# Kernel tuning notes

Hardware: AMD Instinct MI355X
Metric: run time of the kernel (lower is better)

Reference implementation:

```python
import jax, jax.numpy as jnp
import numpy as np

FEATURE_DIM = 4
H_PATCHES = 16
W_PATCHES = 16
PATCH_H = 16
PATCH_W = 16
D = FEATURE_DIM * PATCH_H * PATCH_W  # 1024
N = 2 * H_PATCHES * W_PATCHES        # 512
M = 256
B = 64
EPS = 1e-5


def layernorm(x, g, b):
    mu = jnp.mean(x, axis=-1, keepdims=True)
    var = jnp.var(x, axis=-1, keepdims=True)
    return (x - mu) * jax.lax.rsqrt(var + EPS) * g + b


def box3x3(x):
    # per-channel 3x3 window sum with zero padding == diagonal conv in BCIM
    p = jnp.pad(x, ((0, 0), (0, 0), (1, 1), (1, 1)))
    H, W = x.shape[2], x.shape[3]
    return sum(p[:, :, i:i + H, j:j + W] for i in range(3) for j in range(3))


def setup_inputs() -> dict:
    key = jax.random.key(0)
    ks = jax.random.split(key, 20)
    rn = lambda k, shp, s=0.02: (jax.random.normal(k, shp, dtype=jnp.float32) * s)
    inp = {
        'p_vector': jax.random.normal(ks[0], (B, N, D), dtype=jnp.float32),
        'object_vector': jax.random.normal(ks[1], (M, D), dtype=jnp.float32),
        'ln_p_g': 1.0 + rn(ks[2], (D,), 0.1), 'ln_p_b': rn(ks[3], (D,)),
        'ln_o_g': 1.0 + rn(ks[4], (D,), 0.1), 'ln_o_b': rn(ks[5], (D,)),
        'Wq': rn(ks[6], (D, D)), 'bq': rn(ks[7], (D,)),
        'Wk': rn(ks[8], (D, D)), 'bk': rn(ks[9], (D,)),
        'Wv': rn(ks[10], (D, D)), 'bv': rn(ks[11], (D,)),
        'W1': rn(ks[12], (D, D)), 'b1': rn(ks[13], (D,)),
        'ln1_g': 1.0 + rn(ks[14], (D,), 0.1), 'ln1_b': rn(ks[15], (D,)),
        'W2': rn(ks[16], (D, D)), 'b2': rn(ks[17], (D,)),
        'ln2_g': 1.0 + rn(ks[18], (D,), 0.1), 'ln2_b': rn(ks[19], (D,)),
    }
    return inp


def reference(p_vector, object_vector, ln_p_g, ln_p_b, ln_o_g, ln_o_b,
              Wq, bq, Wk, bk, Wv, bv, W1, b1, ln1_g, ln1_b,
              W2, b2, ln2_g, ln2_b):
    # cross-attention (single head, full D)
    p = layernorm(p_vector, ln_p_g, ln_p_b)            # [B,N,D]
    o = layernorm(object_vector, ln_o_g, ln_o_b)       # [M,D]
    q = jnp.einsum('bnd,de->bne', p, Wq) + bq
    k = o @ Wk + bk                                    # [M,D]
    v = o @ Wv + bv
    A = jax.nn.softmax(jnp.einsum('bnd,md->bnm', q, k), axis=-1)
    p = p + jnp.einsum('bnm,md->bnd', A, v)
    # projection block: Linear->LN->GELU->Linear->LN->GELU, residual
    h = jax.nn.gelu(layernorm(jnp.einsum('bnd,de->bne', p, W1) + b1, ln1_g, ln1_b), approximate=False)
    h = jax.nn.gelu(layernorm(jnp.einsum('bnd,de->bne', h, W2) + b2, ln2_g, ln2_b), approximate=False)
    p = p + h
    # BCIM: reshape to image of 2D channels
    x = jnp.transpose(p, (0, 2, 1)).reshape(B, 2 * D, H_PATCHES, W_PATCHES)
    norm = jnp.linalg.norm(x, axis=1, keepdims=True)
    unit = x / norm
    win = box3x3(unit) / 9.0
    sim = jnp.sum(unit * win, axis=1, keepdims=True)   # [B,1,hp,wp]
    x = x * sim
    # reshape back to [B, 2*hp*wp, D]
    x = jnp.transpose(x, (0, 2, 3, 1)).reshape(B, H_PATCHES, W_PATCHES, D, 2)
    x = jnp.transpose(x, (0, 4, 1, 2, 3)).reshape(B, 2 * H_PATCHES * W_PATCHES, D)
    return x
```

## Files before the change

### kernel.cpp

```cpp
#include <hip/hip_runtime.h>
#include <math.h>

#define D_DIM 1024
#define M_DIM 256
#define B_IMG 64
#define N_TOK 512
#define BN    32768

typedef unsigned short u16;
typedef __attribute__((ext_vector_type(8))) __bf16 bf16x8;
typedef __attribute__((ext_vector_type(4))) float  f32x4;

__device__ __forceinline__ u16 f2bf(float f) {
  union { float f; unsigned u; } c; c.f = f;
  unsigned u = c.u;
  return (u16)((u + 0x7FFFu + ((u >> 16) & 1u)) >> 16);
}
__device__ __forceinline__ float bf2f(u16 h) {
  union { unsigned u; float f; } c; c.u = ((unsigned)h) << 16;
  return c.f;
}

__global__ __launch_bounds__(64) void detect_dtype(const u16* __restrict__ p, int* __restrict__ dflag)
{
  const int lane = threadIdx.x;
  const float a = fabsf(bf2f(p[lane * 2]));
  const bool sane = (a >= 1e-20f && a <= 1e3f);
  const unsigned long long m = __ballot(sane);
  if (lane == 0) *dflag = (m == ~0ull) ? 0 : 1;
}

__device__ __forceinline__ float load_in(const void* p, size_t i, int f) {
  return f ? ((const float*)p)[i] : bf2f(((const u16*)p)[i]);
}

template<int EPI>
__global__ __launch_bounds__(256) void gemm_bt(
    const u16* __restrict__ X0, const u16* __restrict__ X1, const u16* __restrict__ X2,
    const u16* __restrict__ Bt0, const u16* __restrict__ Bt1, const u16* __restrict__ Bt2,
    const void* __restrict__ bias, const int* __restrict__ dflag,
    int np_base, int np_extra,
    const u16* res_hi, const u16* res_lo,
    float* outf, u16* outb, u16* outb2,
    int R, int K, int NC)
{
  __shared__ u16 lA[128 * 64];
  __shared__ u16 lB[128 * 64];
  const int tid  = threadIdx.x;
  const int wave = tid >> 6, lane = tid & 63;
  const int quad = lane >> 4, l15 = lane & 15;
  const int wr = wave & 1, wc = wave >> 1;
  const int rblk = blockIdx.x, cblk = blockIdx.y;

  const int np = np_base + (np_extra ? np_extra * (*dflag) : 0);

  const int srow = lane >> 3;
  const int scol = ((lane & 7) ^ (srow & 7)) * 8;

  const u16* Xs[3] = {X0, X1, X2};
  const u16* Bs[3] = {Bt0, Bt1, Bt2};

  f32x4 acc[4][4] = {};

  for (int p = 0; p < np; ++p) {
    const u16* gA = Xs[p] + (size_t)(rblk * 128 + srow) * K + scol;
    const u16* gB = Bs[p] + (size_t)(cblk * 128 + srow) * K + scol;
    for (int k0 = 0; k0 < K; k0 += 64) {
#pragma unroll
      for (int i = 0; i < 4; ++i) {
        const int j = i * 4 + wave;
        __builtin_amdgcn_global_load_lds(
            (const __attribute__((address_space(1))) void*)(gA + (size_t)j * 8 * K + k0),
            (__attribute__((address_space(3))) void*)(lA + j * 512), 16, 0, 0);
        __builtin_amdgcn_global_load_lds(
            (const __attribute__((address_space(1))) void*)(gB + (size_t)j * 8 * K + k0),
            (__attribute__((address_space(3))) void*)(lB + j * 512), 16, 0, 0);
      }
      __syncthreads();
#pragma unroll
      for (int s = 0; s < 2; ++s) {
        bf16x8 af[4], bfr[4];
#pragma unroll
        for (int r = 0; r < 4; ++r) {
          const int row  = wr * 64 + r * 16 + l15;
          const int slot = (s * 4 + quad) ^ (row & 7);
          af[r] = *(const bf16x8*)(lA + row * 64 + slot * 8);
        }
#pragma unroll
        for (int c = 0; c < 4; ++c) {
          const int row  = wc * 64 + c * 16 + l15;
          const int slot = (s * 4 + quad) ^ (row & 7);
          bfr[c] = *(const bf16x8*)(lB + row * 64 + slot * 8);
        }
#pragma unroll
        for (int r = 0; r < 4; ++r)
#pragma unroll
          for (int c = 0; c < 4; ++c)
            acc[r][c] = __builtin_amdgcn_mfma_f32_16x16x32_bf16(af[r], bfr[c], acc[r][c], 0, 0, 0);
      }
      __syncthreads();
    }
  }

  const int fdt = bias ? *dflag : 0;
  const int crow0 = rblk * 128 + wr * 64;
  const int ccol0 = cblk * 128 + wc * 64;
#pragma unroll
  for (int c = 0; c < 4; ++c) {
    const int col = ccol0 + c * 16 + l15;
    const float bcol = bias ? load_in(bias, col, fdt) : 0.0f;
#pragma unroll
    for (int r = 0; r < 4; ++r) {
#pragma unroll
      for (int t = 0; t < 4; ++t) {
        const int row = crow0 + r * 16 + quad * 4 + t;
        const size_t idx = (size_t)row * NC + col;
        float v = acc[r][c][t] + bcol;
        if (EPI == 0) {
          outb[idx] = f2bf(v);
        } else if (EPI == 1) {
          outf[idx] = v;
        } else if (EPI == 2) {
          const float p = bf2f(res_hi[idx]) + bf2f(res_lo[idx]) + v;
          const u16 hi = f2bf(p);
          outb[idx]  = hi;
          outb2[idx] = f2bf(p - bf2f(hi));
        } else if (EPI == 3) {
          outb[(size_t)col * R + row] = f2bf(v);
        } else {
          const u16 hi = f2bf(v);
          outb[idx]  = hi;
          outb2[idx] = f2bf(v - bf2f(hi));
        }
      }
    }
  }
}

template<int EPI>
__global__ __launch_bounds__(512, 2) void gemm256(
    const u16* __restrict__ X0, const u16* __restrict__ X1, const u16* __restrict__ X2,
    const u16* __restrict__ Bt0, const u16* __restrict__ Bt1, const u16* __restrict__ Bt2,
    const void* __restrict__ bias, const int* __restrict__ dflag,
    int np_base, int np_extra,
    const u16* res_hi, const u16* res_lo,
    float* outf, u16* outb, u16* outb2,
    int R, int K, int NC)
{
  extern __shared__ u16 lds2[];
  const int tid  = threadIdx.x;
  const int wave = tid >> 6, lane = tid & 63;
  const int quad = lane >> 4, l15 = lane & 15;
  const int wm = wave >> 2, wn = wave & 3;
  const int rblk = blockIdx.x, cblk = blockIdx.y;

  const int np = np_base + (np_extra ? np_extra * (*dflag) : 0);
  const int ktiles = K >> 5;
  const int ktl = 31 - __builtin_clz(ktiles);
  const int NT = np << ktl;

  const u16* Xs[3] = {X0, X1, X2};
  const u16* Bs[3] = {Bt0, Bt1, Bt2};

  const int srow  = lane >> 2;
  const int sslot = lane & 3;

  f32x4 acc[8][4] = {};

  auto stage_tile = [&](int t) {
    const int tc = t < NT ? t : NT - 1;
    const int p  = tc >> ktl;
    const int k0 = (tc & (ktiles - 1)) << 5;
    u16* dst = lds2 + (t & 3) * 16384;
#pragma unroll
    for (int i = 0; i < 2; ++i) {
      const int rbase = wave * 32 + i * 16;
      const int r  = rbase + srow;
      const int cg = (sslot ^ ((r >> 1) & 3)) * 8;
      __builtin_amdgcn_global_load_lds(
          (const __attribute__((address_space(1))) void*)(Xs[p] + (size_t)(rblk * 256 + r) * K + k0 + cg),
          (__attribute__((address_space(3))) void*)(dst + rbase * 32), 16, 0, 0);
    }
#pragma unroll
    for (int i = 0; i < 2; ++i) {
      const int rbase = wave * 32 + i * 16;
      const int r  = rbase + srow;
      const int cg = (sslot ^ ((r >> 1) & 3)) * 8;
      __builtin_amdgcn_global_load_lds(
          (const __attribute__((address_space(1))) void*)(Bs[p] + (size_t)(cblk * 256 + r) * K + k0 + cg),
          (__attribute__((address_space(3))) void*)(dst + 8192 + rbase * 32), 16, 0, 0);
    }
  };

  stage_tile(0);
  stage_tile(1);
  asm volatile("s_waitcnt vmcnt(4)" ::: "memory");
  __builtin_amdgcn_s_barrier();

  for (int t = 0; t < NT; ++t) {
    const u16* bufA = lds2 + (t & 3) * 16384;
    const u16* bufB = bufA + 8192;
    bf16x8 bfr[4], af[4];
#pragma unroll
    for (int n = 0; n < 4; ++n) {
      const int row = wn * 64 + n * 16 + l15;
      const int ps  = quad ^ ((row >> 1) & 3);
      bfr[n] = *(const bf16x8*)(bufB + row * 32 + ps * 8);
    }
#pragma unroll
    for (int m = 0; m < 4; ++m) {
      const int row = wm * 128 + m * 16 + l15;
      const int ps  = quad ^ ((row >> 1) & 3);
      af[m] = *(const bf16x8*)(bufA + row * 32 + ps * 8);
    }
    stage_tile(t + 2);
    __builtin_amdgcn_s_barrier();
    asm volatile("s_waitcnt lgkmcnt(0)" ::: "memory");
    __builtin_amdgcn_s_setprio(1);
#pragma unroll
    for (int m = 0; m < 4; ++m)
#pragma unroll
      for (int n = 0; n < 4; ++n)
        acc[m][n] = __builtin_amdgcn_mfma_f32_16x16x32_bf16(af[m], bfr[n], acc[m][n], 0, 0, 0);
    __builtin_amdgcn_s_setprio(0);
    __builtin_amdgcn_s_barrier();
#pragma unroll
    for (int m = 0; m < 4; ++m) {
      const int row = wm * 128 + 64 + m * 16 + l15;
      const int ps  = quad ^ ((row >> 1) & 3);
      af[m] = *(const bf16x8*)(bufA + row * 32 + ps * 8);
    }
    asm volatile("s_waitcnt vmcnt(4)" ::: "memory");
    __builtin_amdgcn_s_barrier();
    asm volatile("s_waitcnt lgkmcnt(0)" ::: "memory");
    __builtin_amdgcn_s_setprio(1);
#pragma unroll
    for (int m = 0; m < 4; ++m)
#pragma unroll
      for (int n = 0; n < 4; ++n)
        acc[4 + m][n] = __builtin_amdgcn_mfma_f32_16x16x32_bf16(af[m], bfr[n], acc[4 + m][n], 0, 0, 0);
    __builtin_amdgcn_s_setprio(0);
    __builtin_amdgcn_s_barrier();
  }

  const int fdt = bias ? *dflag : 0;
  const int crow0 = rblk * 256 + wm * 128;
  const int ccol0 = cblk * 256 + wn * 64;
#pragma unroll
  for (int n = 0; n < 4; ++n) {
    const int col = ccol0 + n * 16 + l15;
    const float bcol = bias ? load_in(bias, col, fdt) : 0.0f;
#pragma unroll
    for (int m = 0; m < 8; ++m) {
#pragma unroll
      for (int u = 0; u < 4; ++u) {
        const int row = crow0 + m * 16 + quad * 4 + u;
        const size_t idx = (size_t)row * NC + col;
        float v = acc[m][n][u] + bcol;
        if (EPI == 0) {
          outb[idx] = f2bf(v);
        } else if (EPI == 1) {
          outf[idx] = v;
        } else if (EPI == 2) {
          const float pp = bf2f(res_hi[idx]) + bf2f(res_lo[idx]) + v;
          const u16 hi = f2bf(pp);
          outb[idx]  = hi;
          outb2[idx] = f2bf(pp - bf2f(hi));
        } else {
          const u16 hi = f2bf(v);
          outb[idx]  = hi;
          outb2[idx] = f2bf(v - bf2f(hi));
        }
      }
    }
  }
}

__global__ __launch_bounds__(256) void ln_row(
    const void* __restrict__ x, const void* __restrict__ g, const void* __restrict__ b,
    const int* __restrict__ dflag, u16* __restrict__ oh, u16* __restrict__ ol)
{
  const int f = *dflag;
  const int row = blockIdx.x, tid = threadIdx.x;
  const int col = tid * 4;
  const size_t base = (size_t)row * 1024 + col;
  float v0, v1, v2, v3;
  if (f) {
    const float4 xv = *(const float4*)((const float*)x + base);
    v0 = xv.x; v1 = xv.y; v2 = xv.z; v3 = xv.w;
  } else {
    const ushort4 xv = *(const ushort4*)((const u16*)x + base);
    v0 = bf2f(xv.x); v1 = bf2f(xv.y); v2 = bf2f(xv.z); v3 = bf2f(xv.w);
  }
  float s  = v0 + v1 + v2 + v3;
  float sq = v0 * v0 + v1 * v1 + v2 * v2 + v3 * v3;
#pragma unroll
  for (int o = 32; o > 0; o >>= 1) { s += __shfl_xor(s, o); sq += __shfl_xor(sq, o); }
  __shared__ float red[8];
  if ((tid & 63) == 0) { red[tid >> 6] = s; red[4 + (tid >> 6)] = sq; }
  __syncthreads();
  s  = red[0] + red[1] + red[2] + red[3];
  sq = red[4] + red[5] + red[6] + red[7];
  const float mean = s * (1.0f / 1024.0f);
  const float var  = sq * (1.0f / 1024.0f) - mean * mean;
  const float rs   = rsqrtf(var + 1e-5f);
  float y[4];
  y[0] = (v0 - mean) * rs * load_in(g, col + 0, f) + load_in(b, col + 0, f);
  y[1] = (v1 - mean) * rs * load_in(g, col + 1, f) + load_in(b, col + 1, f);
  y[2] = (v2 - mean) * rs * load_in(g, col + 2, f) + load_in(b, col + 2, f);
  y[3] = (v3 - mean) * rs * load_in(g, col + 3, f) + load_in(b, col + 3, f);
  ushort4 hv, lv;
  hv.x = f2bf(y[0]); lv.x = f2bf(y[0] - bf2f(hv.x));
  hv.y = f2bf(y[1]); lv.y = f2bf(y[1] - bf2f(hv.y));
  hv.z = f2bf(y[2]); lv.z = f2bf(y[2] - bf2f(hv.z));
  hv.w = f2bf(y[3]); lv.w = f2bf(y[3] - bf2f(hv.w));
  *(ushort4*)(oh + base) = hv;
  *(ushort4*)(ol + base) = lv;
}

template<int MODE>
__global__ __launch_bounds__(256) void ln_gelu(
    const u16* __restrict__ x, const void* __restrict__ g, const void* __restrict__ b,
    const int* __restrict__ dflag,
    const u16* res_hi, const u16* res_lo,
    u16* ob, u16* oh, u16* ol)
{
  const int f = *dflag;
  const int row = blockIdx.x, tid = threadIdx.x;
  const int col = tid * 4;
  const size_t base = (size_t)row * 1024 + col;
  const ushort4 xv = *(const ushort4*)(x + base);
  const float v0 = bf2f(xv.x), v1 = bf2f(xv.y), v2 = bf2f(xv.z), v3 = bf2f(xv.w);
  float s  = v0 + v1 + v2 + v3;
  float sq = v0 * v0 + v1 * v1 + v2 * v2 + v3 * v3;
#pragma unroll
  for (int o = 32; o > 0; o >>= 1) { s += __shfl_xor(s, o); sq += __shfl_xor(sq, o); }
  __shared__ float red[8];
  if ((tid & 63) == 0) { red[tid >> 6] = s; red[4 + (tid >> 6)] = sq; }
  __syncthreads();
  s  = red[0] + red[1] + red[2] + red[3];
  sq = red[4] + red[5] + red[6] + red[7];
  const float mean = s * (1.0f / 1024.0f);
  const float var  = sq * (1.0f / 1024.0f) - mean * mean;
  const float rs   = rsqrtf(var + 1e-5f);
  float z[4], h[4];
  z[0] = (v0 - mean) * rs * load_in(g, col + 0, f) + load_in(b, col + 0, f);
  z[1] = (v1 - mean) * rs * load_in(g, col + 1, f) + load_in(b, col + 1, f);
  z[2] = (v2 - mean) * rs * load_in(g, col + 2, f) + load_in(b, col + 2, f);
  z[3] = (v3 - mean) * rs * load_in(g, col + 3, f) + load_in(b, col + 3, f);
#pragma unroll
  for (int i = 0; i < 4; ++i)
    h[i] = 0.5f * z[i] * (1.0f + erff(z[i] * 0.70710678118654752f));
  if (MODE == 0) {
    *(ushort4*)(ob + base) = make_ushort4(f2bf(h[0]), f2bf(h[1]), f2bf(h[2]), f2bf(h[3]));
  } else {
    const ushort4 rh = *(const ushort4*)(res_hi + base);
    const ushort4 rl = *(const ushort4*)(res_lo + base);
    float p[4];
    p[0] = bf2f(rh.x) + bf2f(rl.x) + h[0];
    p[1] = bf2f(rh.y) + bf2f(rl.y) + h[1];
    p[2] = bf2f(rh.z) + bf2f(rl.z) + h[2];
    p[3] = bf2f(rh.w) + bf2f(rl.w) + h[3];
    ushort4 hv, lv;
    hv.x = f2bf(p[0]); lv.x = f2bf(p[0] - bf2f(hv.x));
    hv.y = f2bf(p[1]); lv.y = f2bf(p[1] - bf2f(hv.y));
    hv.z = f2bf(p[2]); lv.z = f2bf(p[2] - bf2f(hv.z));
    hv.w = f2bf(p[3]); lv.w = f2bf(p[3] - bf2f(hv.w));
    *(ushort4*)(oh + base) = hv;
    *(ushort4*)(ol + base) = lv;
  }
}

__global__ __launch_bounds__(256) void softmax256(const float* __restrict__ S, u16* __restrict__ A)
{
  const int tid = threadIdx.x, lane = tid & 63, wave = tid >> 6;
  const size_t row = (size_t)blockIdx.x * 4 + wave;
  const float4 v = *(const float4*)(S + row * 256 + lane * 4);
  float m = fmaxf(fmaxf(v.x, v.y), fmaxf(v.z, v.w));
#pragma unroll
  for (int o = 32; o > 0; o >>= 1) m = fmaxf(m, __shfl_xor(m, o));
  const float e0 = expf(v.x - m), e1 = expf(v.y - m), e2 = expf(v.z - m), e3 = expf(v.w - m);
  float s = e0 + e1 + e2 + e3;
#pragma unroll
  for (int o = 32; o > 0; o >>= 1) s += __shfl_xor(s, o);
  const float r = 1.0f / s;
  *(ushort4*)(A + row * 256 + lane * 4) =
      make_ushort4(f2bf(e0 * r), f2bf(e1 * r), f2bf(e2 * r), f2bf(e3 * r));
}

__global__ __launch_bounds__(256) void wtrans5(
    const void* w0, const void* w1, const void* w2, const void* w3, const void* w4,
    u16* h0, u16* h1, u16* h2, u16* h3, u16* h4,
    u16* l0, u16* l1, u16* l2, u16* l3, u16* l4,
    const int* __restrict__ dflag)
{
  const int f = *dflag;
  const void* W; u16* H; u16* L;
  switch (blockIdx.z) {
    case 0: W = w0; H = h0; L = l0; break;
    case 1: W = w1; H = h1; L = l1; break;
    case 2: W = w2; H = h2; L = l2; break;
    case 3: W = w3; H = h3; L = l3; break;
    default: W = w4; H = h4; L = l4; break;
  }
  __shared__ u16 th[32][33];
  __shared__ u16 tl[32][33];
  const int tx = threadIdx.x & 31, ty = threadIdx.x >> 5;
  const int bx = blockIdx.x, by = blockIdx.y;
#pragma unroll
  for (int i = 0; i < 4; ++i) {
    const int r = ty + i * 8;
    const float v = load_in(W, ((size_t)by * 32 + r) * 1024 + bx * 32 + tx, f);
    const u16 hi = f2bf(v);
    th[r][tx] = hi;
    tl[r][tx] = f2bf(v - bf2f(hi));
  }
  __syncthreads();
#pragma unroll
  for (int i = 0; i < 4; ++i) {
    const int r = ty + i * 8;
    const size_t o = ((size_t)bx * 32 + r) * 1024 + by * 32 + tx;
    H[o] = th[tx][r];
    L[o] = tl[tx][r];
  }
}

__global__ __launch_bounds__(256) void zerof(float* p, int n)
{
  const int i = blockIdx.x * 256 + threadIdx.x;
  if (i < n) p[i] = 0.0f;
}

__global__ __launch_bounds__(256) void bcim_dots(
    const u16* __restrict__ p2h, const u16* __restrict__ p2l, float* __restrict__ G)
{
  const int b = blockIdx.x, ds = blockIdx.y;
  __shared__ float T[512][17];
  float acc[9] = {0, 0, 0, 0, 0, 0, 0, 0, 0};
  const int tid = threadIdx.x;
  const int px = tid & 15, py = tid >> 4;
  for (int ch = 0; ch < 8; ++ch) {
    const int d0 = ds * 128 + ch * 16;
#pragma unroll
    for (int i = 0; i < 8; ++i) {
      const int j = i * 256 + tid;
      const int r = j >> 2, q4 = j & 3;
      const size_t base = ((size_t)b * 512 + r) * 1024 + d0 + q4 * 4;
      const ushort4 hv = *(const ushort4*)(p2h + base);
      const ushort4 lv = *(const ushort4*)(p2l + base);
      T[r][q4 * 4 + 0] = bf2f(hv.x) + bf2f(lv.x);
      T[r][q4 * 4 + 1] = bf2f(hv.y) + bf2f(lv.y);
      T[r][q4 * 4 + 2] = bf2f(hv.z) + bf2f(lv.z);
      T[r][q4 * 4 + 3] = bf2f(hv.w) + bf2f(lv.w);
    }
    __syncthreads();
    float a0[16], a1[16];
#pragma unroll
    for (int dc = 0; dc < 16; ++dc) { a0[dc] = T[tid][dc]; a1[dc] = T[tid + 256][dc]; }
#pragma unroll
    for (int o = 0; o < 9; ++o) {
      const int dy = o / 3 - 1, dx = o % 3 - 1;
      const int qx = px + dx, qy = py + dy;
      if (qx >= 0 && qx < 16 && qy >= 0 && qy < 16) {
        const int qp = qy * 16 + qx;
        float sum = 0.0f;
#pragma unroll
        for (int dc = 0; dc < 16; ++dc)
          sum += a0[dc] * T[qp][dc] + a1[dc] * T[qp + 256][dc];
        acc[o] += sum;
      }
    }
    __syncthreads();
  }
#pragma unroll
  for (int o = 0; o < 9; ++o)
    atomicAdd(&G[((size_t)b * 9 + o) * 256 + tid], acc[o]);
}

__global__ __launch_bounds__(256) void bcim_sim_k(const float* __restrict__ G, float* __restrict__ sim)
{
  const int b = blockIdx.x, tid = threadIdx.x;
  __shared__ float nrm[256];
  const float nv = sqrtf(G[((size_t)b * 9 + 4) * 256 + tid]);
  nrm[tid] = nv;
  __syncthreads();
  const int px = tid & 15, py = tid >> 4;
  float s = 0.0f;
#pragma unroll
  for (int o = 0; o < 9; ++o) {
    const int dy = o / 3 - 1, dx = o % 3 - 1;
    const int qx = px + dx, qy = py + dy;
    if (qx >= 0 && qx < 16 && qy >= 0 && qy < 16)
      s += G[((size_t)b * 9 + o) * 256 + tid] / (nv * nrm[qy * 16 + qx]);
  }
  sim[b * 256 + tid] = s * (1.0f / 9.0f);
}

__global__ __launch_bounds__(256) void bcim_scale(
    const u16* __restrict__ p2h, const u16* __restrict__ p2l,
    const float* __restrict__ sim, float* __restrict__ out)
{
  const size_t i4 = (size_t)blockIdx.x * 256 + threadIdx.x;
  const size_t base = i4 * 4;
  const ushort4 hv = *(const ushort4*)(p2h + base);
  const ushort4 lv = *(const ushort4*)(p2l + base);
  const size_t n = base >> 10;
  const size_t b = n >> 9;
  const int pix = (int)(n & 255);
  const float s = sim[b * 256 + pix];
  *(float4*)(out + base) = make_float4(
      (bf2f(hv.x) + bf2f(lv.x)) * s, (bf2f(hv.y) + bf2f(lv.y)) * s,
      (bf2f(hv.z) + bf2f(lv.z)) * s, (bf2f(hv.w) + bf2f(lv.w)) * s);
}

extern "C" void kernel_launch(void* const* d_in, const int* in_sizes, int n_in,
                              void* d_out, int out_size, void* d_ws, size_t ws_size,
                              hipStream_t stream)
{
  (void)in_sizes; (void)n_in; (void)out_size; (void)ws_size;
  const void* p_vector      = d_in[0];
  const void* object_vector = d_in[1];
  const void* ln_p_g = d_in[2];
  const void* ln_p_b = d_in[3];
  const void* ln_o_g = d_in[4];
  const void* ln_o_b = d_in[5];
  const void* Wq = d_in[6];  const void* bq = d_in[7];
  const void* Wk = d_in[8];  const void* bk = d_in[9];
  const void* Wv = d_in[10]; const void* bv = d_in[11];
  const void* W1 = d_in[12]; const void* b1 = d_in[13];
  const void* ln1_g = d_in[14]; const void* ln1_b = d_in[15];
  const void* W2 = d_in[16]; const void* b2 = d_in[17];
  const void* ln2_g = d_in[18]; const void* ln2_b = d_in[19];
  float* out = (float*)d_out;

  char* ws = (char*)d_ws;
  size_t off = 0;
  auto alloc = [&](size_t bytes) -> void* {
    void* p = ws + off;
    off += (bytes + 255) & ~(size_t)255;
    return p;
  };
  int* dflag = (int*)alloc(256);
  u16* WqH = (u16*)alloc((size_t)D_DIM * D_DIM * 2);
  u16* WkH = (u16*)alloc((size_t)D_DIM * D_DIM * 2);
  u16* WvH = (u16*)alloc((size_t)D_DIM * D_DIM * 2);
  u16* W1H = (u16*)alloc((size_t)D_DIM * D_DIM * 2);
  u16* W2H = (u16*)alloc((size_t)D_DIM * D_DIM * 2);
  u16* WqL = (u16*)alloc((size_t)D_DIM * D_DIM * 2);
  u16* WkL = (u16*)alloc((size_t)D_DIM * D_DIM * 2);
  u16* WvL = (u16*)alloc((size_t)D_DIM * D_DIM * 2);
  u16* W1L = (u16*)alloc((size_t)D_DIM * D_DIM * 2);
  u16* W2L = (u16*)alloc((size_t)D_DIM * D_DIM * 2);
  u16* PH = (u16*)alloc((size_t)BN * D_DIM * 2);
  u16* PL = (u16*)alloc((size_t)BN * D_DIM * 2);
  u16* QH = (u16*)alloc((size_t)BN * D_DIM * 2);
  u16* QL = (u16*)alloc((size_t)BN * D_DIM * 2);
  float* S_f = (float*)alloc((size_t)BN * M_DIM * 4);
  u16* A_b   = (u16*)alloc((size_t)BN * M_DIM * 2);
  u16* onH = (u16*)alloc((size_t)M_DIM * D_DIM * 2);
  u16* onL = (u16*)alloc((size_t)M_DIM * D_DIM * 2);
  u16* kH  = (u16*)alloc((size_t)M_DIM * D_DIM * 2);
  u16* kL  = (u16*)alloc((size_t)M_DIM * D_DIM * 2);
  u16* vT  = (u16*)alloc((size_t)D_DIM * M_DIM * 2);
  float* G   = (float*)alloc((size_t)B_IMG * 9 * 256 * 4);
  float* sim = (float*)alloc((size_t)B_IMG * 256 * 4);

  detect_dtype<<<1, 64, 0, stream>>>((const u16*)p_vector, dflag);
  wtrans5<<<dim3(32, 32, 5), 256, 0, stream>>>(Wq, Wk, Wv, W1, W2,
      WqH, WkH, WvH, W1H, W2H, WqL, WkL, WvL, W1L, W2L, dflag);
  zerof<<<(B_IMG * 9 * 256 + 255) / 256, 256, 0, stream>>>(G, B_IMG * 9 * 256);

  ln_row<<<BN, 256, 0, stream>>>(p_vector, ln_p_g, ln_p_b, dflag, PH, PL);
  ln_row<<<M_DIM, 256, 0, stream>>>(object_vector, ln_o_g, ln_o_b, dflag, onH, onL);

  gemm_bt<4><<<dim3(2, 8), 256, 0, stream>>>(onH, onL, onH, WkH, WkH, WkL,
      bk, dflag, 2, 1, nullptr, nullptr, nullptr, kH, kL, M_DIM, D_DIM, D_DIM);
  gemm_bt<3><<<dim3(2, 8), 256, 0, stream>>>(onH, onL, onH, WvH, WvH, WvL,
      bv, dflag, 2, 1, nullptr, nullptr, nullptr, vT, nullptr, M_DIM, D_DIM, D_DIM);
  gemm256<4><<<dim3(128, 4), 512, 131072, stream>>>(PH, PL, PH, WqH, WqH, WqL,
      bq, dflag, 2, 1, nullptr, nullptr, nullptr, QH, QL, BN, D_DIM, D_DIM);

  gemm_bt<1><<<dim3(256, 2), 256, 0, stream>>>(QH, QL, QH, kH, kH, kL,
      nullptr, dflag, 3, 0, nullptr, nullptr, S_f, nullptr, nullptr, BN, D_DIM, M_DIM);
  softmax256<<<BN / 4, 256, 0, stream>>>(S_f, A_b);

  gemm256<2><<<dim3(128, 4), 512, 131072, stream>>>(A_b, nullptr, nullptr, vT, nullptr, nullptr,
      nullptr, dflag, 1, 0, PH, PL, nullptr, PH, PL, BN, M_DIM, D_DIM);

  gemm256<0><<<dim3(128, 4), 512, 131072, stream>>>(PH, nullptr, nullptr, W1H, nullptr, nullptr,
      b1, dflag, 1, 0, nullptr, nullptr, nullptr, QH, nullptr, BN, D_DIM, D_DIM);
  ln_gelu<0><<<BN, 256, 0, stream>>>(QH, ln1_g, ln1_b, dflag, nullptr, nullptr, QL, nullptr, nullptr);

  gemm256<0><<<dim3(128, 4), 512, 131072, stream>>>(QL, nullptr, nullptr, W2H, nullptr, nullptr,
      b2, dflag, 1, 0, nullptr, nullptr, nullptr, QH, nullptr, BN, D_DIM, D_DIM);
  ln_gelu<1><<<BN, 256, 0, stream>>>(QH, ln2_g, ln2_b, dflag, PH, PL, nullptr, PH, PL);

  bcim_dots<<<dim3(B_IMG, 8), 256, 0, stream>>>(PH, PL, G);
  bcim_sim_k<<<B_IMG, 256, 0, stream>>>(G, sim);
  bcim_scale<<<(BN * D_DIM / 4) / 256, 256, 0, stream>>>(PH, PL, sim, out);
}
```

Before: 1.565 ms.

## Fuse K/V GEMMs, deepen gemm256 prefetch, swap grid order, use gemm_bt for single-pass GEMMs

Merges the separate K and V projection GEMMs into one launch that picks its weights by blockIdx.z. The 256x256 GEMM now prefetches three tiles ahead instead of two, and its grid is transposed so consecutive blocks share the same row panel of A. The single-pass GEMMs (A·V, W1, W2) now use the smaller 128-tile gemm_bt kernel instead of gemm256. The goal is less launch overhead, better latency hiding and better L2 reuse. The deeper prefetch uses all four LDS buffers, which raises the risk of a WAR hazard on the buffer still being read.

After: 1.385 ms. -11.5%, faster.

```diff
diff --git a/kernel.cpp b/kernel.cpp
--- a/kernel.cpp
+++ b/kernel.cpp
@@ -137,6 +137,103 @@
   }
 }
 
+__global__ __launch_bounds__(256) void gemm_kv(
+    const u16* __restrict__ on_h, const u16* __restrict__ on_l,
+    const u16* __restrict__ WkH_, const u16* __restrict__ WkL_,
+    const u16* __restrict__ WvH_, const u16* __restrict__ WvL_,
+    const void* __restrict__ bk_, const void* __restrict__ bv_,
+    const int* __restrict__ dflag,
+    u16* __restrict__ kh, u16* __restrict__ kl, u16* __restrict__ vt)
+{
+  __shared__ u16 lA[128 * 64];
+  __shared__ u16 lB[128 * 64];
+  const int tid  = threadIdx.x;
+  const int wave = tid >> 6, lane = tid & 63;
+  const int quad = lane >> 4, l15 = lane & 15;
+  const int wr = wave & 1, wc = wave >> 1;
+  const int rblk = blockIdx.x, cblk = blockIdx.y;
+  const int zv = blockIdx.z;
+  const int K = D_DIM, NC = D_DIM, R = M_DIM;
+
+  const int np = 2 + *dflag;
+
+  const int srow = lane >> 3;
+  const int scol = ((lane & 7) ^ (srow & 7)) * 8;
+
+  const u16* Xs[3] = {on_h, on_l, on_h};
+  const u16* Bs[3];
+  if (zv == 0) { Bs[0] = WkH_; Bs[1] = WkH_; Bs[2] = WkL_; }
+  else         { Bs[0] = WvH_; Bs[1] = WvH_; Bs[2] = WvL_; }
+  const void* bias = zv == 0 ? bk_ : bv_;
+
+  f32x4 acc[4][4] = {};
+
+  for (int p = 0; p < np; ++p) {
+    const u16* gA = Xs[p] + (size_t)(rblk * 128 + srow) * K + scol;
+    const u16* gB = Bs[p] + (size_t)(cblk * 128 + srow) * K + scol;
+    for (int k0 = 0; k0 < K; k0 += 64) {
+#pragma unroll
+      for (int i = 0; i < 4; ++i) {
+        const int j = i * 4 + wave;
+        __builtin_amdgcn_global_load_lds(
+            (const __attribute__((address_space(1))) void*)(gA + (size_t)j * 8 * K + k0),
+            (__attribute__((address_space(3))) void*)(lA + j * 512), 16, 0, 0);
+        __builtin_amdgcn_global_load_lds(
+            (const __attribute__((address_space(1))) void*)(gB + (size_t)j * 8 * K + k0),
+            (__attribute__((address_space(3))) void*)(lB + j * 512), 16, 0, 0);
+      }
+      __syncthreads();
+#pragma unroll
+      for (int s = 0; s < 2; ++s) {
+        bf16x8 af[4], bfr[4];
+#pragma unroll
+        for (int r = 0; r < 4; ++r) {
+          const int row  = wr * 64 + r * 16 + l15;
+          const int slot = (s * 4 + quad) ^ (row & 7);
+          af[r] = *(const bf16x8*)(lA + row * 64 + slot * 8);
+        }
+#pragma unroll
+        for (int c = 0; c < 4; ++c) {
+          const int row  = wc * 64 + c * 16 + l15;
+          const int slot = (s * 4 + quad) ^ (row & 7);
+          bfr[c] = *(const bf16x8*)(lB + row * 64 + slot * 8);
+        }
+#pragma unroll
+        for (int r = 0; r < 4; ++r)
+#pragma unroll
+          for (int c = 0; c < 4; ++c)
+            acc[r][c] = __builtin_amdgcn_mfma_f32_16x16x32_bf16(af[r], bfr[c], acc[r][c], 0, 0, 0);
+      }
+      __syncthreads();
+    }
+  }
+
+  const int fdt = *dflag;
+  const int crow0 = rblk * 128 + wr * 64;
+  const int ccol0 = cblk * 128 + wc * 64;
+#pragma unroll
+  for (int c = 0; c < 4; ++c) {
+    const int col = ccol0 + c * 16 + l15;
+    const float bcol = load_in(bias, col, fdt);
+#pragma unroll
+    for (int r = 0; r < 4; ++r) {
+#pragma unroll
+      for (int t = 0; t < 4; ++t) {
+        const int row = crow0 + r * 16 + quad * 4 + t;
+        float v = acc[r][c][t] + bcol;
+        if (zv == 0) {
+          const size_t idx = (size_t)row * NC + col;
+          const u16 hi = f2bf(v);
+          kh[idx] = hi;
+          kl[idx] = f2bf(v - bf2f(hi));
+        } else {
+          vt[(size_t)col * R + row] = f2bf(v);
+        }
+      }
+    }
+  }
+}
+
 template<int EPI>
 __global__ __launch_bounds__(512, 2) void gemm256(
     const u16* __restrict__ X0, const u16* __restrict__ X1, const u16* __restrict__ X2,
@@ -152,7 +249,7 @@
   const int wave = tid >> 6, lane = tid & 63;
   const int quad = lane >> 4, l15 = lane & 15;
   const int wm = wave >> 2, wn = wave & 3;
-  const int rblk = blockIdx.x, cblk = blockIdx.y;
+  const int rblk = blockIdx.y, cblk = blockIdx.x;
 
   const int np = np_base + (np_extra ? np_extra * (*dflag) : 0);
   const int ktiles = K >> 5;
@@ -194,7 +291,8 @@
 
   stage_tile(0);
   stage_tile(1);
-  asm volatile("s_waitcnt vmcnt(4)" ::: "memory");
+  stage_tile(2);
+  asm volatile("s_waitcnt vmcnt(8)" ::: "memory");
   __builtin_amdgcn_s_barrier();
 
   for (int t = 0; t < NT; ++t) {
@@ -213,7 +311,7 @@
       const int ps  = quad ^ ((row >> 1) & 3);
       af[m] = *(const bf16x8*)(bufA + row * 32 + ps * 8);
     }
-    stage_tile(t + 2);
+    stage_tile(t + 3);
     __builtin_amdgcn_s_barrier();
     asm volatile("s_waitcnt lgkmcnt(0)" ::: "memory");
     __builtin_amdgcn_s_setprio(1);
@@ -230,7 +328,7 @@
       const int ps  = quad ^ ((row >> 1) & 3);
       af[m] = *(const bf16x8*)(bufA + row * 32 + ps * 8);
     }
-    asm volatile("s_waitcnt vmcnt(4)" ::: "memory");
+    asm volatile("s_waitcnt vmcnt(8)" ::: "memory");
     __builtin_amdgcn_s_barrier();
     asm volatile("s_waitcnt lgkmcnt(0)" ::: "memory");
     __builtin_amdgcn_s_setprio(1);
@@ -242,6 +340,7 @@
     __builtin_amdgcn_s_setprio(0);
     __builtin_amdgcn_s_barrier();
   }
+  asm volatile("s_waitcnt vmcnt(0)" ::: "memory");
 
   const int fdt = bias ? *dflag : 0;
   const int crow0 = rblk * 256 + wm * 128;
@@ -573,25 +672,23 @@
   ln_row<<<BN, 256, 0, stream>>>(p_vector, ln_p_g, ln_p_b, dflag, PH, PL);
   ln_row<<<M_DIM, 256, 0, stream>>>(object_vector, ln_o_g, ln_o_b, dflag, onH, onL);
 
-  gemm_bt<4><<<dim3(2, 8), 256, 0, stream>>>(onH, onL, onH, WkH, WkH, WkL,
-      bk, dflag, 2, 1, nullptr, nullptr, nullptr, kH, kL, M_DIM, D_DIM, D_DIM);
-  gemm_bt<3><<<dim3(2, 8), 256, 0, stream>>>(onH, onL, onH, WvH, WvH, WvL,
-      bv, dflag, 2, 1, nullptr, nullptr, nullptr, vT, nullptr, M_DIM, D_DIM, D_DIM);
-  gemm256<4><<<dim3(128, 4), 512, 131072, stream>>>(PH, PL, PH, WqH, WqH, WqL,
+  gemm_kv<<<dim3(2, 8, 2), 256, 0, stream>>>(onH, onL, WkH, WkL, WvH, WvL,
+      bk, bv, dflag, kH, kL, vT);
+  gemm256<4><<<dim3(4, 128), 512, 131072, stream>>>(PH, PL, PH, WqH, WqH, WqL,
       bq, dflag, 2, 1, nullptr, nullptr, nullptr, QH, QL, BN, D_DIM, D_DIM);
 
   gemm_bt<1><<<dim3(256, 2), 256, 0, stream>>>(QH, QL, QH, kH, kH, kL,
       nullptr, dflag, 3, 0, nullptr, nullptr, S_f, nullptr, nullptr, BN, D_DIM, M_DIM);
   softmax256<<<BN / 4, 256, 0, stream>>>(S_f, A_b);
 
-  gemm256<2><<<dim3(128, 4), 512, 131072, stream>>>(A_b, nullptr, nullptr, vT, nullptr, nullptr,
+  gemm_bt<2><<<dim3(256, 8), 256, 0, stream>>>(A_b, nullptr, nullptr, vT, nullptr, nullptr,
       nullptr, dflag, 1, 0, PH, PL, nullptr, PH, PL, BN, M_DIM, D_DIM);
 
-  gemm256<0><<<dim3(128, 4), 512, 131072, stream>>>(PH, nullptr, nullptr, W1H, nullptr, nullptr,
+  gemm_bt<0><<<dim3(256, 8), 256, 0, stream>>>(PH, nullptr, nullptr, W1H, nullptr, nullptr,
       b1, dflag, 1, 0, nullptr, nullptr, nullptr, QH, nullptr, BN, D_DIM, D_DIM);
   ln_gelu<0><<<BN, 256, 0, stream>>>(QH, ln1_g, ln1_b, dflag, nullptr, nullptr, QL, nullptr, nullptr);
 
-  gemm256<0><<<dim3(128, 4), 512, 131072, stream>>>(QL, nullptr, nullptr, W2H, nullptr, nullptr,
+  gemm_bt<0><<<dim3(256, 8), 256, 0, stream>>>(QL, nullptr, nullptr, W2H, nullptr, nullptr,
       b2, dflag, 1, 0, nullptr, nullptr, nullptr, QH, nullptr, BN, D_DIM, D_DIM);
   ln_gelu<1><<<BN, 256, 0, stream>>>(QH, ln2_g, ln2_b, dflag, PH, PL, nullptr, PH, PL);
 
```
